# Performance work log

Measured on AMD Instinct MI355X. Metric: run time of the kernel, lower is better.

The kernel has to match this reference:

```python
import jax, jax.numpy as jnp
import numpy as np

N = 131072
H = 768

def setup_inputs() -> dict:
    key = jax.random.key(0)
    k1, k2, k3, k4 = jax.random.split(key, 4)
    h_i = jax.random.normal(k1, (N, H), dtype=jnp.float32)
    W_weight = jax.random.normal(k2, (H, H), dtype=jnp.float32) * 0.02
    W_bias = jax.random.normal(k3, (H,), dtype=jnp.float32) * 0.02
    v = jax.random.normal(k4, (1, H), dtype=jnp.float32) * 0.1
    return {"h_i": h_i, "W_weight": W_weight, "W_bias": W_bias, "v": v}

def reference(h_i, W_weight, W_bias, v):
    # u_i = tanh(Linear(h_i)) : [N, H]
    u_i = jnp.tanh(h_i @ W_weight.T + W_bias)
    # scores = v @ u_i.T : [1, N]
    scores = v @ u_i.T
    alpha = jax.nn.softmax(scores, axis=1)  # [1, N]
    # weighted sum over N -> [1, H]
    return alpha @ h_i
```

## Files before the change

### kernel.cpp

```cpp
#include <hip/hip_runtime.h>

#define HDIM 768
#define BM 64
#define NCHUNK 24
#define CHALF 24576
#define A_STRIDE 1552

typedef _Float16 f16x8 __attribute__((ext_vector_type(8)));
typedef _Float16 f16x4 __attribute__((ext_vector_type(4)));
typedef _Float16 f16x2 __attribute__((ext_vector_type(2)));
typedef float f32x4 __attribute__((ext_vector_type(4)));

#define LDS_A     0
#define LDS_BIAS  99328
#define LDS_V     102400
#define LDS_SRED  105472
#define LDS_E     109568
#define LDS_TOTAL 109824

#define WS_WT    0
#define WS_Z     1179648
#define WS_PART  1179712
#define WS_PART2 7471168
#define WS_NEED  (WS_PART2 + 49152)

__device__ __forceinline__ float tanh_fast(float z) {
    float e2 = __expf(2.0f * z);
    return 1.0f - 2.0f / (e2 + 1.0f);
}

__device__ __forceinline__ f16x8 cvt8(f32x4 x0, f32x4 x1) {
    f16x8 f;
    f[0] = (_Float16)x0[0]; f[1] = (_Float16)x0[1];
    f[2] = (_Float16)x0[2]; f[3] = (_Float16)x0[3];
    f[4] = (_Float16)x1[0]; f[5] = (_Float16)x1[1];
    f[6] = (_Float16)x1[2]; f[7] = (_Float16)x1[3];
    return f;
}

__global__ __launch_bounds__(1024) void prep_kernel(
    const float* __restrict__ W, _Float16* __restrict__ Wt,
    float* __restrict__ Z, float* __restrict__ accbuf) {
    int idx = blockIdx.x * 1024 + threadIdx.x;
    if (idx < 73728) {
        int c  = idx / 96;
        int r  = idx - c * 96;
        int kc = r >> 2;
        int q  = r & 3;
        const float* src = W + c * HDIM + kc * 32 + q * 8;
        f16x8 v = cvt8(*(const f32x4*)src, *(const f32x4*)(src + 4));
        *(f16x8*)(Wt + (size_t)kc * CHALF + c * 32 + q * 8) = v;
    }
    if (idx < HDIM) accbuf[idx] = 0.0f;
    if (idx == 0) *Z = 0.0f;
}

__global__ __launch_bounds__(1024, 4) void score_fused_kernel(
    const float* __restrict__ h, const _Float16* __restrict__ Wt,
    const float* __restrict__ bias, const float* __restrict__ vvec,
    float* __restrict__ part, float* __restrict__ accbuf,
    float* __restrict__ Z, int use_part) {

    extern __shared__ char smem[];
    float* bias_s = (float*)(smem + LDS_BIAS);
    float* v_s    = (float*)(smem + LDS_V);
    float* s_red  = (float*)(smem + LDS_SRED);
    float* e_lds  = (float*)(smem + LDS_E);

    const int tid  = threadIdx.x;
    const int wave = tid >> 6;
    const int lane = tid & 63;
    const int l15  = lane & 15;
    const int lhi  = lane >> 4;
    const int row0 = blockIdx.x * BM;

    if (tid < HDIM) { bias_s[tid] = bias[tid]; v_s[tid] = vvec[tid]; }

    #pragma unroll
    for (int i = 0; i < 12; ++i) {
        int flat = i * 1024 + tid;
        int r  = flat / 192;
        int c4 = flat - r * 192;
        f32x4 x = __builtin_nontemporal_load(
            (const f32x4*)(h + (size_t)(row0 + r) * HDIM + c4 * 4));
        f16x4 v;
        v[0] = (_Float16)x[0]; v[1] = (_Float16)x[1];
        v[2] = (_Float16)x[2]; v[3] = (_Float16)x[3];
        *(f16x4*)(smem + LDS_A + r * A_STRIDE + c4 * 8) = v;
    }

    const _Float16* wcur = Wt + (wave * 48 + l15) * 32 + lhi * 8;
    f16x8 bA0 = *(const f16x8*)(wcur);
    f16x8 bA1 = *(const f16x8*)(wcur + 512);
    f16x8 bA2 = *(const f16x8*)(wcur + 1024);
    f16x8 bB0, bB1, bB2;

    __syncthreads();

    f32x4 acc[4][3];
    #pragma unroll
    for (int rt = 0; rt < 4; ++rt)
        #pragma unroll
        for (int ct = 0; ct < 3; ++ct)
            acc[rt][ct] = (f32x4){0.f, 0.f, 0.f, 0.f};

    const char* aBase = smem + LDS_A + l15 * A_STRIDE + lhi * 16;

#define CHUNK(KOFF, PF, BC0, BC1, BC2, BN0, BN1, BN2)                                    \
    {                                                                                    \
        const _Float16* wn = wcur + (PF) * CHALF;                                        \
        BN0 = *(const f16x8*)(wn);                                                       \
        BN1 = *(const f16x8*)(wn + 512);                                                 \
        BN2 = *(const f16x8*)(wn + 1024);                                                \
        const char* ab = aBase + (KOFF);                                                 \
        f16x8 a0 = *(const f16x8*)(ab);                                                  \
        f16x8 a1 = *(const f16x8*)(ab + 16 * A_STRIDE);                                  \
        f16x8 a2 = *(const f16x8*)(ab + 32 * A_STRIDE);                                  \
        f16x8 a3 = *(const f16x8*)(ab + 48 * A_STRIDE);                                  \
        acc[0][0] = __builtin_amdgcn_mfma_f32_16x16x32_f16(a0, BC0, acc[0][0], 0, 0, 0); \
        acc[0][1] = __builtin_amdgcn_mfma_f32_16x16x32_f16(a0, BC1, acc[0][1], 0, 0, 0); \
        acc[0][2] = __builtin_amdgcn_mfma_f32_16x16x32_f16(a0, BC2, acc[0][2], 0, 0, 0); \
        acc[1][0] = __builtin_amdgcn_mfma_f32_16x16x32_f16(a1, BC0, acc[1][0], 0, 0, 0); \
        acc[1][1] = __builtin_amdgcn_mfma_f32_16x16x32_f16(a1, BC1, acc[1][1], 0, 0, 0); \
        acc[1][2] = __builtin_amdgcn_mfma_f32_16x16x32_f16(a1, BC2, acc[1][2], 0, 0, 0); \
        acc[2][0] = __builtin_amdgcn_mfma_f32_16x16x32_f16(a2, BC0, acc[2][0], 0, 0, 0); \
        acc[2][1] = __builtin_amdgcn_mfma_f32_16x16x32_f16(a2, BC1, acc[2][1], 0, 0, 0); \
        acc[2][2] = __builtin_amdgcn_mfma_f32_16x16x32_f16(a2, BC2, acc[2][2], 0, 0, 0); \
        acc[3][0] = __builtin_amdgcn_mfma_f32_16x16x32_f16(a3, BC0, acc[3][0], 0, 0, 0); \
        acc[3][1] = __builtin_amdgcn_mfma_f32_16x16x32_f16(a3, BC1, acc[3][1], 0, 0, 0); \
        acc[3][2] = __builtin_amdgcn_mfma_f32_16x16x32_f16(a3, BC2, acc[3][2], 0, 0, 0); \
    }

    #pragma unroll 1
    for (int k2 = 0; k2 < NCHUNK; k2 += 2) {
        CHUNK(k2 * 64,      1, bA0, bA1, bA2, bB0, bB1, bB2)
        CHUNK(k2 * 64 + 64, 2, bB0, bB1, bB2, bA0, bA1, bA2)
        wcur += 2 * CHALF;
    }
#undef CHUNK

    float pr[4][4];
    #pragma unroll
    for (int rt = 0; rt < 4; ++rt)
        #pragma unroll
        for (int r = 0; r < 4; ++r) pr[rt][r] = 0.f;

    #pragma unroll
    for (int ct = 0; ct < 3; ++ct) {
        int col = wave * 48 + ct * 16 + l15;
        float bj = bias_s[col];
        float vj = v_s[col];
        #pragma unroll
        for (int rt = 0; rt < 4; ++rt)
            #pragma unroll
            for (int r = 0; r < 4; ++r)
                pr[rt][r] = fmaf(vj, tanh_fast(acc[rt][ct][r] + bj), pr[rt][r]);
    }
    #pragma unroll
    for (int rt = 0; rt < 4; ++rt)
        #pragma unroll
        for (int r = 0; r < 4; ++r) {
            float x = pr[rt][r];
            x += __shfl_xor(x, 1);
            x += __shfl_xor(x, 2);
            x += __shfl_xor(x, 4);
            x += __shfl_xor(x, 8);
            if (l15 == 0) s_red[wave * 64 + rt * 16 + lhi * 4 + r] = x;
        }
    __syncthreads();

    if (tid < 64) {
        float s = 0.f;
        #pragma unroll
        for (int w = 0; w < 16; ++w) s += s_red[w * 64 + tid];
        float e = __expf(s);
        e_lds[tid] = e;
        float tot = e;
        tot += __shfl_xor(tot, 1);
        tot += __shfl_xor(tot, 2);
        tot += __shfl_xor(tot, 4);
        tot += __shfl_xor(tot, 8);
        tot += __shfl_xor(tot, 16);
        tot += __shfl_xor(tot, 32);
        if (tid == 0) atomicAdd(Z, tot);
    }
    __syncthreads();

    if (tid < 384) {
        float s0 = 0.f, s1 = 0.f;
        #pragma unroll 8
        for (int i = 0; i < BM; ++i) {
            f16x2 a2 = *(const f16x2*)(smem + LDS_A + i * A_STRIDE + tid * 4);
            float e = e_lds[i];
            s0 = fmaf(e, (float)a2[0], s0);
            s1 = fmaf(e, (float)a2[1], s1);
        }
        if (use_part) {
            float* dst = part + (size_t)blockIdx.x * HDIM + tid * 2;
            dst[0] = s0; dst[1] = s1;
        } else {
            atomicAdd(accbuf + tid * 2, s0);
            atomicAdd(accbuf + tid * 2 + 1, s1);
        }
    }
}

__global__ __launch_bounds__(128) void fin1_kernel(
    const float* __restrict__ part, float* __restrict__ part2) {
    const int g  = blockIdx.x / 6;
    const int cb = blockIdx.x % 6;
    const int col = cb * 128 + threadIdx.x;
    float s = 0.f;
    #pragma unroll 8
    for (int p = g * 128; p < (g + 1) * 128; ++p) s += part[(size_t)p * HDIM + col];
    part2[g * HDIM + col] = s;
}

__global__ __launch_bounds__(128) void fin2_kernel(
    const float* __restrict__ src, const float* __restrict__ Z,
    float* __restrict__ out, int ngroups) {
    const int col = blockIdx.x * 128 + threadIdx.x;
    float s = 0.f;
    for (int g = 0; g < ngroups; ++g) s += src[g * HDIM + col];
    out[col] = s / (*Z);
}

extern "C" void kernel_launch(void* const* d_in, const int* in_sizes, int n_in,
                              void* d_out, int out_size, void* d_ws, size_t ws_size,
                              hipStream_t stream) {
    const float* h    = (const float*)d_in[0];
    const float* W    = (const float*)d_in[1];
    const float* bias = (const float*)d_in[2];
    const float* vv   = (const float*)d_in[3];
    float* out = (float*)d_out;

    const int n = in_sizes[0] / HDIM;

    char* ws = (char*)d_ws;
    _Float16* Wt  = (_Float16*)(ws + WS_WT);
    float* Z      = (float*)(ws + WS_Z);
    float* part   = (float*)(ws + WS_PART);
    float* part2  = (float*)(ws + WS_PART2);
    float* accbuf = (float*)(ws + WS_PART);

    const int use_part = (ws_size >= (size_t)WS_NEED) ? 1 : 0;

    hipFuncSetAttribute((const void*)score_fused_kernel,
                        hipFuncAttributeMaxDynamicSharedMemorySize, LDS_TOTAL);

    prep_kernel<<<72, 1024, 0, stream>>>(W, Wt, Z, accbuf);

    score_fused_kernel<<<n / BM, 1024, LDS_TOTAL, stream>>>(
        h, Wt, bias, vv, part, accbuf, Z, use_part);

    if (use_part) {
        fin1_kernel<<<96, 128, 0, stream>>>(part, part2);
        fin2_kernel<<<HDIM / 128, 128, 0, stream>>>(part2, Z, out, 16);
    } else {
        fin2_kernel<<<HDIM / 128, 128, 0, stream>>>(accbuf, Z, out, 1);
    }
}
```

Before: 288.8 us.

## Halve score-kernel row tile to 32 and drop manual weight prefetch

After: 331.8 us. 1.15x slower.

```diff
diff --git a/kernel.cpp b/kernel.cpp
--- a/kernel.cpp
+++ b/kernel.cpp
@@ -1,7 +1,7 @@
 #include <hip/hip_runtime.h>
 
 #define HDIM 768
-#define BM 64
+#define BM 32
 #define NCHUNK 24
 #define CHALF 24576
 #define A_STRIDE 1552
@@ -12,17 +12,17 @@
 typedef float f32x4 __attribute__((ext_vector_type(4)));
 
 #define LDS_A     0
-#define LDS_BIAS  99328
-#define LDS_V     102400
-#define LDS_SRED  105472
-#define LDS_E     109568
-#define LDS_TOTAL 109824
+#define LDS_BIAS  49664
+#define LDS_V     52736
+#define LDS_SRED  55808
+#define LDS_E     57856
+#define LDS_TOTAL 57984
 
 #define WS_WT    0
 #define WS_Z     1179648
 #define WS_PART  1179712
-#define WS_PART2 7471168
-#define WS_NEED  (WS_PART2 + 49152)
+#define WS_PART2 13762624
+#define WS_NEED  (WS_PART2 + 98304)
 
 __device__ __forceinline__ float tanh_fast(float z) {
     float e2 = __expf(2.0f * z);
@@ -55,7 +55,7 @@
     if (idx == 0) *Z = 0.0f;
 }
 
-__global__ __launch_bounds__(1024, 4) void score_fused_kernel(
+__global__ __launch_bounds__(1024) void score_fused_kernel(
     const float* __restrict__ h, const _Float16* __restrict__ Wt,
     const float* __restrict__ bias, const float* __restrict__ vvec,
     float* __restrict__ part, float* __restrict__ accbuf,
@@ -77,7 +77,7 @@
     if (tid < HDIM) { bias_s[tid] = bias[tid]; v_s[tid] = vvec[tid]; }
 
     #pragma unroll
-    for (int i = 0; i < 12; ++i) {
+    for (int i = 0; i < 6; ++i) {
         int flat = i * 1024 + tid;
         int r  = flat / 192;
         int c4 = flat - r * 192;
@@ -88,60 +88,38 @@
         v[2] = (_Float16)x[2]; v[3] = (_Float16)x[3];
         *(f16x4*)(smem + LDS_A + r * A_STRIDE + c4 * 8) = v;
     }
-
-    const _Float16* wcur = Wt + (wave * 48 + l15) * 32 + lhi * 8;
-    f16x8 bA0 = *(const f16x8*)(wcur);
-    f16x8 bA1 = *(const f16x8*)(wcur + 512);
-    f16x8 bA2 = *(const f16x8*)(wcur + 1024);
-    f16x8 bB0, bB1, bB2;
-
     __syncthreads();
 
-    f32x4 acc[4][3];
-    #pragma unroll
-    for (int rt = 0; rt < 4; ++rt)
+    f32x4 acc[2][3];
+    #pragma unroll
+    for (int rt = 0; rt < 2; ++rt)
         #pragma unroll
         for (int ct = 0; ct < 3; ++ct)
             acc[rt][ct] = (f32x4){0.f, 0.f, 0.f, 0.f};
 
+    const _Float16* wtp = Wt + (wave * 48 + l15) * 32 + lhi * 8;
     const char* aBase = smem + LDS_A + l15 * A_STRIDE + lhi * 16;
 
-#define CHUNK(KOFF, PF, BC0, BC1, BC2, BN0, BN1, BN2)                                    \
-    {                                                                                    \
-        const _Float16* wn = wcur + (PF) * CHALF;                                        \
-        BN0 = *(const f16x8*)(wn);                                                       \
-        BN1 = *(const f16x8*)(wn + 512);                                                 \
-        BN2 = *(const f16x8*)(wn + 1024);                                                \
-        const char* ab = aBase + (KOFF);                                                 \
-        f16x8 a0 = *(const f16x8*)(ab);                                                  \
-        f16x8 a1 = *(const f16x8*)(ab + 16 * A_STRIDE);                                  \
-        f16x8 a2 = *(const f16x8*)(ab + 32 * A_STRIDE);                                  \
-        f16x8 a3 = *(const f16x8*)(ab + 48 * A_STRIDE);                                  \
-        acc[0][0] = __builtin_amdgcn_mfma_f32_16x16x32_f16(a0, BC0, acc[0][0], 0, 0, 0); \
-        acc[0][1] = __builtin_amdgcn_mfma_f32_16x16x32_f16(a0, BC1, acc[0][1], 0, 0, 0); \
-        acc[0][2] = __builtin_amdgcn_mfma_f32_16x16x32_f16(a0, BC2, acc[0][2], 0, 0, 0); \
-        acc[1][0] = __builtin_amdgcn_mfma_f32_16x16x32_f16(a1, BC0, acc[1][0], 0, 0, 0); \
-        acc[1][1] = __builtin_amdgcn_mfma_f32_16x16x32_f16(a1, BC1, acc[1][1], 0, 0, 0); \
-        acc[1][2] = __builtin_amdgcn_mfma_f32_16x16x32_f16(a1, BC2, acc[1][2], 0, 0, 0); \
-        acc[2][0] = __builtin_amdgcn_mfma_f32_16x16x32_f16(a2, BC0, acc[2][0], 0, 0, 0); \
-        acc[2][1] = __builtin_amdgcn_mfma_f32_16x16x32_f16(a2, BC1, acc[2][1], 0, 0, 0); \
-        acc[2][2] = __builtin_amdgcn_mfma_f32_16x16x32_f16(a2, BC2, acc[2][2], 0, 0, 0); \
-        acc[3][0] = __builtin_amdgcn_mfma_f32_16x16x32_f16(a3, BC0, acc[3][0], 0, 0, 0); \
-        acc[3][1] = __builtin_amdgcn_mfma_f32_16x16x32_f16(a3, BC1, acc[3][1], 0, 0, 0); \
-        acc[3][2] = __builtin_amdgcn_mfma_f32_16x16x32_f16(a3, BC2, acc[3][2], 0, 0, 0); \
-    }
-
-    #pragma unroll 1
-    for (int k2 = 0; k2 < NCHUNK; k2 += 2) {
-        CHUNK(k2 * 64,      1, bA0, bA1, bA2, bB0, bB1, bB2)
-        CHUNK(k2 * 64 + 64, 2, bB0, bB1, bB2, bA0, bA1, bA2)
-        wcur += 2 * CHALF;
-    }
-#undef CHUNK
-
-    float pr[4][4];
-    #pragma unroll
-    for (int rt = 0; rt < 4; ++rt)
+    #pragma unroll 2
+    for (int kc = 0; kc < NCHUNK; ++kc) {
+        const _Float16* wp = wtp + (size_t)kc * CHALF;
+        f16x8 b0 = *(const f16x8*)(wp);
+        f16x8 b1 = *(const f16x8*)(wp + 512);
+        f16x8 b2 = *(const f16x8*)(wp + 1024);
+        const char* ab = aBase + kc * 64;
+        f16x8 a0 = *(const f16x8*)(ab);
+        f16x8 a1 = *(const f16x8*)(ab + 16 * A_STRIDE);
+        acc[0][0] = __builtin_amdgcn_mfma_f32_16x16x32_f16(a0, b0, acc[0][0], 0, 0, 0);
+        acc[0][1] = __builtin_amdgcn_mfma_f32_16x16x32_f16(a0, b1, acc[0][1], 0, 0, 0);
+        acc[0][2] = __builtin_amdgcn_mfma_f32_16x16x32_f16(a0, b2, acc[0][2], 0, 0, 0);
+        acc[1][0] = __builtin_amdgcn_mfma_f32_16x16x32_f16(a1, b0, acc[1][0], 0, 0, 0);
+        acc[1][1] = __builtin_amdgcn_mfma_f32_16x16x32_f16(a1, b1, acc[1][1], 0, 0, 0);
+        acc[1][2] = __builtin_amdgcn_mfma_f32_16x16x32_f16(a1, b2, acc[1][2], 0, 0, 0);
+    }
+
+    float pr[2][4];
+    #pragma unroll
+    for (int rt = 0; rt < 2; ++rt)
         #pragma unroll
         for (int r = 0; r < 4; ++r) pr[rt][r] = 0.f;
 
@@ -151,13 +129,13 @@
         float bj = bias_s[col];
         float vj = v_s[col];
         #pragma unroll
-        for (int rt = 0; rt < 4; ++rt)
+        for (int rt = 0; rt < 2; ++rt)
             #pragma unroll
             for (int r = 0; r < 4; ++r)
                 pr[rt][r] = fmaf(vj, tanh_fast(acc[rt][ct][r] + bj), pr[rt][r]);
     }
     #pragma unroll
-    for (int rt = 0; rt < 4; ++rt)
+    for (int rt = 0; rt < 2; ++rt)
         #pragma unroll
         for (int r = 0; r < 4; ++r) {
             float x = pr[rt][r];
@@ -165,14 +143,14 @@
             x += __shfl_xor(x, 2);
             x += __shfl_xor(x, 4);
             x += __shfl_xor(x, 8);
-            if (l15 == 0) s_red[wave * 64 + rt * 16 + lhi * 4 + r] = x;
+            if (l15 == 0) s_red[wave * 32 + rt * 16 + lhi * 4 + r] = x;
         }
     __syncthreads();
 
-    if (tid < 64) {
+    if (tid < 32) {
         float s = 0.f;
         #pragma unroll
-        for (int w = 0; w < 16; ++w) s += s_red[w * 64 + tid];
+        for (int w = 0; w < 16; ++w) s += s_red[w * 32 + tid];
         float e = __expf(s);
         e_lds[tid] = e;
         float tot = e;
@@ -181,7 +159,6 @@
         tot += __shfl_xor(tot, 4);
         tot += __shfl_xor(tot, 8);
         tot += __shfl_xor(tot, 16);
-        tot += __shfl_xor(tot, 32);
         if (tid == 0) atomicAdd(Z, tot);
     }
     __syncthreads();
@@ -254,8 +231,8 @@
         h, Wt, bias, vv, part, accbuf, Z, use_part);
 
     if (use_part) {
-        fin1_kernel<<<96, 128, 0, stream>>>(part, part2);
-        fin2_kernel<<<HDIM / 128, 128, 0, stream>>>(part2, Z, out, 16);
+        fin1_kernel<<<192, 128, 0, stream>>>(part, part2);
+        fin2_kernel<<<HDIM / 128, 128, 0, stream>>>(part2, Z, out, 32);
     } else {
         fin2_kernel<<<HDIM / 128, 128, 0, stream>>>(accbuf, Z, out, 1);
     }
```
